# Kernel tuning notes

Hardware: AMD Instinct MI355X
Metric: run time of the kernel (lower is better)

## Reference

```python
import jax, jax.numpy as jnp
import numpy as np

EMBED = 768
HEADS = 12
D_K = EMBED // HEADS  # 64


def setup_inputs() -> dict:
    key = jax.random.key(0)
    ks = jax.random.split(key, 9)
    w_scale = EMBED ** -0.5
    inp = {
        "x": jax.random.normal(ks[0], (128, 256, 1, EMBED), dtype=jnp.float32),
        "Wq": jax.random.normal(ks[1], (EMBED, EMBED), dtype=jnp.float32) * w_scale,
        "bq": jax.random.normal(ks[2], (EMBED,), dtype=jnp.float32) * 0.02,
        "Wk": jax.random.normal(ks[3], (EMBED, EMBED), dtype=jnp.float32) * w_scale,
        "bk": jax.random.normal(ks[4], (EMBED,), dtype=jnp.float32) * 0.02,
        "Wv": jax.random.normal(ks[5], (EMBED, EMBED), dtype=jnp.float32) * w_scale,
        "bv": jax.random.normal(ks[6], (EMBED,), dtype=jnp.float32) * 0.02,
        "Wo": jax.random.normal(ks[7], (EMBED, EMBED), dtype=jnp.float32) * w_scale,
        "bo": jax.random.normal(ks[8], (EMBED,), dtype=jnp.float32) * 0.02,
    }
    return inp


def reference(x, Wq, bq, Wk, bk, Wv, bv, Wo, bo):
    # x: (n_rows r, n_cols i/j, batch n, embed)
    R, C, B, E = x.shape
    H, Dk = HEADS, D_K
    # tied-row scaling: d_k^{-1/2} / sqrt(n_rows)
    scaling = (Dk ** -0.5) / np.sqrt(R).astype(np.float32)

    q = (x @ Wq.T + bq).reshape(R, C, B, H, Dk) * scaling
    k = (x @ Wk.T + bk).reshape(R, C, B, H, Dk)
    v = (x @ Wv.T + bv).reshape(R, C, B, H, Dk)

    # scores summed over rows r and head dim d -> (h, n, i, j)
    scores = jnp.einsum('rinhd,rjnhd->hnij', q, k)
    probs = jax.nn.softmax(scores, axis=-1)  # dropout p=0 -> identity

    # shared attention applied per row
    c = jnp.einsum('hnij,rjnhd->rinhd', probs, v).reshape(R, C, B, E)
    out = c @ Wo.T + bo
    return (out, probs)
```

## Files before the change

kernel.cpp:

```cpp
#include <hip/hip_runtime.h>
#include <math.h>

typedef short bf16x8 __attribute__((ext_vector_type(8)));
typedef float f32x4 __attribute__((ext_vector_type(4)));
typedef unsigned short ushort8 __attribute__((ext_vector_type(8)));
typedef unsigned short ushort4v __attribute__((ext_vector_type(4)));

constexpr int R = 128, Cc = 256, E = 768, H = 12;
constexpr int M = R * Cc;
constexpr size_t TOK = (size_t)M * E;

__device__ __forceinline__ unsigned short f2b(float f) {
  unsigned int u = __float_as_uint(f);
  u += 0x7fff + ((u >> 16) & 1);
  return (unsigned short)(u >> 16);
}

__device__ __forceinline__ void ldst16(const unsigned short* g, unsigned short* l) {
  __builtin_amdgcn_global_load_lds(
      (const __attribute__((address_space(1))) unsigned int*)g,
      (__attribute__((address_space(3))) unsigned int*)l, 16, 0, 0);
}

__global__ __launch_bounds__(256) void cvt_bf16(const float* __restrict__ in,
                                                unsigned short* __restrict__ out,
                                                int n8) {
  int i = blockIdx.x * 256 + threadIdx.x;
  if (i >= n8) return;
  const float4* p = (const float4*)in;
  float4 a = p[2 * i], b = p[2 * i + 1];
  ushort8 o;
  o[0] = f2b(a.x); o[1] = f2b(a.y); o[2] = f2b(a.z); o[3] = f2b(a.w);
  o[4] = f2b(b.x); o[5] = f2b(b.y); o[6] = f2b(b.z); o[7] = f2b(b.w);
  ((ushort8*)out)[i] = o;
}

__global__ __launch_bounds__(256) void cvt_w4(const float* __restrict__ W0,
                                              const float* __restrict__ W1,
                                              const float* __restrict__ W2,
                                              const float* __restrict__ W3,
                                              unsigned short* __restrict__ out) {
  const int region = blockIdx.x / 288;
  const int i = (blockIdx.x % 288) * 256 + threadIdx.x;
  if (i >= 73728) return;
  const float* src = region == 0 ? W0 : (region == 1 ? W1 : (region == 2 ? W2 : W3));
  const float4* p = (const float4*)src;
  float4 a = p[2 * i], b = p[2 * i + 1];
  ushort8 o;
  o[0] = f2b(a.x); o[1] = f2b(a.y); o[2] = f2b(a.z); o[3] = f2b(a.w);
  o[4] = f2b(b.x); o[5] = f2b(b.y); o[6] = f2b(b.z); o[7] = f2b(b.w);
  ((ushort8*)(out + (size_t)region * 589824))[i] = o;
}

__device__ __forceinline__ void stage64(const unsigned short* __restrict__ A, int lda,
                                        const unsigned short* __restrict__ B, int ldb,
                                        int k0, unsigned short* As, unsigned short* Bs,
                                        int wv, int ln, int srow, int scol) {
#pragma unroll
  for (int t = 0; t < 4; ++t) {
    const int ch = wv * 4 + t;
    const int row = ch * 8 + srow;
    ldst16(A + (size_t)row * lda + k0 + scol, As + ch * 512 + ln * 8);
    ldst16(B + (size_t)row * ldb + k0 + scol, Bs + ch * 512 + ln * 8);
  }
}

__device__ __forceinline__ void gemm128(const unsigned short* __restrict__ A, int lda,
                                        const unsigned short* __restrict__ B, int ldb,
                                        int K, unsigned short* As, unsigned short* Bs,
                                        int wv, int ln, int wm, int wn,
                                        f32x4 (&acc)[4][4]) {
  const int srow = ln >> 3;
  const int scol = ((ln & 7) ^ srow) * 8;
  const int nt = K >> 6;
  stage64(A, lda, B, ldb, 0, As, Bs, wv, ln, srow, scol);
  if (nt > 1)
    stage64(A, lda, B, ldb, 64, As + 8192, Bs + 8192, wv, ln, srow, scol);
  for (int t = 0; t < nt; ++t) {
    const int cur = t & 1;
    if (t + 1 < nt) {
      asm volatile("s_waitcnt vmcnt(8)" ::: "memory");
    } else {
      asm volatile("s_waitcnt vmcnt(0)" ::: "memory");
    }
    __builtin_amdgcn_sched_barrier(0);
    __builtin_amdgcn_s_barrier();
    const unsigned short* Ab = As + cur * 8192;
    const unsigned short* Bb = Bs + cur * 8192;
    bf16x8 a[2][4], b[2][4];
    {
      const int rc0 = (((ln >> 4)) ^ (ln & 7)) * 8;
#pragma unroll
      for (int i = 0; i < 4; ++i)
        a[0][i] = *(const bf16x8*)(Ab + (wm + i * 16 + (ln & 15)) * 64 + rc0);
#pragma unroll
      for (int j = 0; j < 4; ++j)
        b[0][j] = *(const bf16x8*)(Bb + (wn + j * 16 + (ln & 15)) * 64 + rc0);
    }
    __builtin_amdgcn_sched_barrier(0);
    {
      const int rc1 = ((4 + (ln >> 4)) ^ (ln & 7)) * 8;
#pragma unroll
      for (int i = 0; i < 4; ++i)
        a[1][i] = *(const bf16x8*)(Ab + (wm + i * 16 + (ln & 15)) * 64 + rc1);
#pragma unroll
      for (int j = 0; j < 4; ++j)
        b[1][j] = *(const bf16x8*)(Bb + (wn + j * 16 + (ln & 15)) * 64 + rc1);
    }
    asm volatile("s_waitcnt lgkmcnt(8)" ::: "memory");
    __builtin_amdgcn_sched_barrier(0);
    __builtin_amdgcn_s_setprio(1);
#pragma unroll
    for (int i = 0; i < 4; ++i)
#pragma unroll
      for (int j = 0; j < 4; ++j)
        acc[i][j] = __builtin_amdgcn_mfma_f32_16x16x32_bf16(a[0][i], b[0][j],
                                                            acc[i][j], 0, 0, 0);
    __builtin_amdgcn_s_setprio(0);
    asm volatile("s_waitcnt lgkmcnt(0)" ::: "memory");
    __builtin_amdgcn_sched_barrier(0);
    __builtin_amdgcn_s_barrier();
    if (t + 2 < nt)
      stage64(A, lda, B, ldb, (t + 2) * 64, As + cur * 8192, Bs + cur * 8192,
              wv, ln, srow, scol);
    __builtin_amdgcn_s_setprio(1);
#pragma unroll
    for (int i = 0; i < 4; ++i)
#pragma unroll
      for (int j = 0; j < 4; ++j)
        acc[i][j] = __builtin_amdgcn_mfma_f32_16x16x32_bf16(a[1][i], b[1][j],
                                                            acc[i][j], 0, 0, 0);
    __builtin_amdgcn_s_setprio(0);
  }
}

__global__ __launch_bounds__(256) void qkv_proj(
    const unsigned short* __restrict__ A, const unsigned short* __restrict__ B,
    const float* __restrict__ bq, const float* __restrict__ bk,
    const float* __restrict__ bv, unsigned short* __restrict__ q2,
    unsigned short* __restrict__ k2, unsigned short* __restrict__ v3, float scaling) {
  __shared__ unsigned short As[2 * 128 * 64];
  __shared__ unsigned short Bs[2 * 128 * 64];
  const int tid = threadIdx.x, wv = tid >> 6, ln = tid & 63;
  const unsigned p = blockIdx.x + blockIdx.y * 18;
  const unsigned l = (p & 7) * 576 + (p >> 3);
  const int bx = l % 18, by = l / 18;
  const int n0 = bx * 128, m0 = by * 128;
  const int wm = (wv & 1) * 64, wn = (wv >> 1) * 64;
  f32x4 acc[4][4] = {};
  gemm128(A + (size_t)m0 * 768, 768, B + (size_t)n0 * 768, 768, 768,
          As, Bs, wv, ln, wm, wn, acc);

  const int region = bx / 6;
  const float* bias = region == 0 ? bq : (region == 1 ? bk : bv);
  const float sc = region == 0 ? scaling : 1.0f;
  const int nq0 = n0 - region * 768;
#pragma unroll
  for (int j = 0; j < 4; ++j) {
    const int np = nq0 + wn + j * 16 + (ln & 15);
    const int h = np >> 6, d = np & 63;
    const float bn = bias[np];
#pragma unroll
    for (int i = 0; i < 4; ++i) {
      const int mb = m0 + wm + i * 16 + (ln >> 4) * 4;
      if (region < 2) {
        unsigned short* dst = region == 0 ? q2 : k2;
#pragma unroll
        for (int r = 0; r < 4; ++r) {
          const int m = mb + r;
          const int ic = m & 255, rr = m >> 8;
          dst[(size_t)h * 2097152 + (size_t)ic * 8192 + rr * 64 + d] =
              f2b((acc[i][j][r] + bn) * sc);
        }
      } else {
        const int jc = mb & 255, rr = mb >> 8;
        ushort4v o;
#pragma unroll
        for (int r = 0; r < 4; ++r) o[r] = f2b(acc[i][j][r] + bn);
        *(ushort4v*)(v3 + (size_t)h * 2097152 + ((size_t)rr * 64 + d) * 256 + jc) = o;
      }
    }
  }
}

__global__ __launch_bounds__(256) void qk_gemm(const unsigned short* __restrict__ q2,
                                               const unsigned short* __restrict__ k2,
                                               float* __restrict__ Sp) {
  __shared__ unsigned short As[2 * 128 * 64];
  __shared__ unsigned short Bs[2 * 128 * 64];
  const int tid = threadIdx.x, wv = tid >> 6, ln = tid & 63;
  const int i0 = (blockIdx.x & 1) * 128, j0 = (blockIdx.x >> 1) * 128;
  const int h = blockIdx.y, kc = blockIdx.z;
  const int wm = (wv & 1) * 64, wn = (wv >> 1) * 64;
  f32x4 acc[4][4] = {};
  const unsigned short* Ap = q2 + (size_t)h * 2097152 + (size_t)i0 * 8192 + kc * 1024;
  const unsigned short* Bp = k2 + (size_t)h * 2097152 + (size_t)j0 * 8192 + kc * 1024;
  gemm128(Ap, 8192, Bp, 8192, 1024, As, Bs, wv, ln, wm, wn, acc);
  float* out = Sp + ((size_t)kc * H + h) * 65536;
#pragma unroll
  for (int j = 0; j < 4; ++j) {
    const int jj = j0 + wn + j * 16 + (ln & 15);
#pragma unroll
    for (int i = 0; i < 4; ++i)
#pragma unroll
      for (int r = 0; r < 4; ++r) {
        const int ii = i0 + wm + i * 16 + (ln >> 4) * 4 + r;
        out[(size_t)ii * 256 + jj] = acc[i][j][r];
      }
  }
}

__global__ __launch_bounds__(256) void softmax_k(const float* __restrict__ Sp,
                                                 float* __restrict__ P,
                                                 unsigned short* __restrict__ Pb) {
  const int row = blockIdx.x, j = threadIdx.x;
  const size_t stride = (size_t)H * Cc * Cc;
  const size_t base = (size_t)row * Cc + j;
  float s = 0.f;
#pragma unroll
  for (int c = 0; c < 8; ++c) s += Sp[base + c * stride];
  float m = s;
#pragma unroll
  for (int o = 32; o > 0; o >>= 1) m = fmaxf(m, __shfl_xor(m, o));
  __shared__ float sm[4], ss[4];
  const int wid = j >> 6, lane = j & 63;
  if (lane == 0) sm[wid] = m;
  __syncthreads();
  m = fmaxf(fmaxf(sm[0], sm[1]), fmaxf(sm[2], sm[3]));
  float e = expf(s - m);
  float t = e;
#pragma unroll
  for (int o = 32; o > 0; o >>= 1) t += __shfl_xor(t, o);
  if (lane == 0) ss[wid] = t;
  __syncthreads();
  t = ss[0] + ss[1] + ss[2] + ss[3];
  const float p = e / t;
  P[base] = p;
  Pb[base] = f2b(p);
}

__global__ __launch_bounds__(256) void pv_gemm(const unsigned short* __restrict__ P,
                                               const unsigned short* __restrict__ V,
                                               unsigned short* __restrict__ Co) {
  __shared__ unsigned short As[2 * 128 * 64];
  __shared__ unsigned short Bs[2 * 128 * 64];
  const int tid = threadIdx.x, wv = tid >> 6, ln = tid & 63;
  const unsigned p = blockIdx.x + blockIdx.y * 128;
  const unsigned l = (p & 7) * 192 + (p >> 3);
  const int bx = l & 127, h = l >> 7;
  const int i0 = (bx & 1) * 128, n0 = (bx >> 1) * 128;
  const int wm = (wv & 1) * 64, wn = (wv >> 1) * 64;
  f32x4 acc[4][4] = {};
  const unsigned short* Ap = P + (size_t)h * 65536 + (size_t)i0 * 256;
  const unsigned short* Bp = V + (size_t)h * 2097152 + (size_t)n0 * 256;
  gemm128(Ap, 256, Bp, 256, 256, As, Bs, wv, ln, wm, wn, acc);
#pragma unroll
  for (int j = 0; j < 4; ++j) {
    const int n = n0 + wn + j * 16 + (ln & 15);
    const int rr = n >> 6, d = n & 63;
#pragma unroll
    for (int i = 0; i < 4; ++i)
#pragma unroll
      for (int r = 0; r < 4; ++r) {
        const int ii = i0 + wm + i * 16 + (ln >> 4) * 4 + r;
        Co[((size_t)rr * 256 + ii) * 768 + h * 64 + d] = f2b(acc[i][j][r]);
      }
  }
}

__global__ __launch_bounds__(256) void o_proj(const unsigned short* __restrict__ A,
                                              const unsigned short* __restrict__ B,
                                              const float* __restrict__ bias,
                                              float* __restrict__ Y) {
  __shared__ unsigned short As[2 * 128 * 64];
  __shared__ unsigned short Bs[2 * 128 * 64];
  const int tid = threadIdx.x, wv = tid >> 6, ln = tid & 63;
  const unsigned p = blockIdx.x + blockIdx.y * 6;
  const unsigned l = (p & 7) * 192 + (p >> 3);
  const int bx = l % 6, by = l / 6;
  const int n0 = bx * 128, m0 = by * 128;
  const int wm = (wv & 1) * 64, wn = (wv >> 1) * 64;
  f32x4 acc[4][4] = {};
  gemm128(A + (size_t)m0 * 768, 768, B + (size_t)n0 * 768, 768, 768,
          As, Bs, wv, ln, wm, wn, acc);
#pragma unroll
  for (int j = 0; j < 4; ++j) {
    const int n = n0 + wn + j * 16 + (ln & 15);
    const float bn = bias[n];
#pragma unroll
    for (int i = 0; i < 4; ++i)
#pragma unroll
      for (int r = 0; r < 4; ++r) {
        const int m = m0 + wm + i * 16 + (ln >> 4) * 4 + r;
        Y[(size_t)m * 768 + n] = acc[i][j][r] + bn;
      }
  }
}

extern "C" void kernel_launch(void* const* d_in, const int* in_sizes, int n_in,
                              void* d_out, int out_size, void* d_ws, size_t ws_size,
                              hipStream_t stream) {
  const float* x  = (const float*)d_in[0];
  const float* Wq = (const float*)d_in[1];
  const float* bq = (const float*)d_in[2];
  const float* Wk = (const float*)d_in[3];
  const float* bk = (const float*)d_in[4];
  const float* Wv = (const float*)d_in[5];
  const float* bv = (const float*)d_in[6];
  const float* Wo = (const float*)d_in[7];
  const float* bo = (const float*)d_in[8];
  float* out = (float*)d_out;
  float* probs = out + TOK;

  char* ws = (char*)d_ws;
  unsigned short* x_bf  = (unsigned short*)(ws);
  unsigned short* q2    = (unsigned short*)(ws + 50331648);
  unsigned short* k2    = (unsigned short*)(ws + 100663296);
  unsigned short* v3    = (unsigned short*)(ws + 150994944);
  unsigned short* Wq_bf = (unsigned short*)(ws + 201326592);
  unsigned short* Wk_bf = Wq_bf + 589824;
  unsigned short* Wv_bf = Wk_bf + 589824;
  unsigned short* Wo_bf = Wv_bf + 589824;
  float* S_part         = (float*)(ws);
  unsigned short* P_bf  = (unsigned short*)(ws + 25165824);
  unsigned short* c_bf  = q2;

  const float scaling = 0.125f / sqrtf(128.f);

  cvt_bf16<<<12288, 256, 0, stream>>>(x, x_bf, 3145728);
  cvt_w4<<<1152, 256, 0, stream>>>(Wq, Wk, Wv, Wo, Wq_bf);

  qkv_proj<<<dim3(18, 256), 256, 0, stream>>>(x_bf, Wq_bf, bq, bk, bv,
                                              q2, k2, v3, scaling);

  qk_gemm<<<dim3(4, H, 8), 256, 0, stream>>>(q2, k2, S_part);
  softmax_k<<<H * Cc, 256, 0, stream>>>(S_part, probs, P_bf);
  pv_gemm<<<dim3(128, H), 256, 0, stream>>>(P_bf, v3, c_bf);

  o_proj<<<dim3(6, 256), 256, 0, stream>>>(c_bf, Wo_bf, bo, out);
}
```

Baseline: 505.0 us.

## Use 256x256 tiles with 512-thread blocks for projection and PV GEMMs

Adds a gemm256 path in which 8 waves compute a 256x256 output tile with a K-step of 32, double-buffered through global_load_lds. The QKV projection, PV and output projection kernels move to it, which doubles operand reuse per byte loaded and reduces the number of blocks. The older gemm128, still used by qk_gemm, is simplified so that all fragment loads complete before a single MFMA phase, dropping the split lgkmcnt overlap. Risks include higher register pressure with 32 accumulators per wave, fewer blocks for load balancing, and possible LDS bank conflicts from the new swizzle.

Result: slower. 528.5 us (+4.7%).

```diff
diff --git a/kernel.cpp b/kernel.cpp
--- a/kernel.cpp
+++ b/kernel.cpp
@@ -50,6 +50,62 @@
   o[0] = f2b(a.x); o[1] = f2b(a.y); o[2] = f2b(a.z); o[3] = f2b(a.w);
   o[4] = f2b(b.x); o[5] = f2b(b.y); o[6] = f2b(b.z); o[7] = f2b(b.w);
   ((ushort8*)(out + (size_t)region * 589824))[i] = o;
+}
+
+__device__ __forceinline__ void stage256(const unsigned short* __restrict__ A, int lda,
+                                         const unsigned short* __restrict__ B, int ldb,
+                                         int k0, unsigned short* As, unsigned short* Bs,
+                                         int tid) {
+  const int r0 = tid >> 2;
+  const int g = ((tid & 3) ^ ((tid >> 3) & 3)) * 8;
+#pragma unroll
+  for (int o = 0; o < 2; ++o) {
+    const int row = o * 128 + r0;
+    ldst16(A + (size_t)row * lda + k0 + g, As + o * 4096 + tid * 8);
+    ldst16(B + (size_t)row * ldb + k0 + g, Bs + o * 4096 + tid * 8);
+  }
+}
+
+__device__ __forceinline__ void gemm256(const unsigned short* __restrict__ A, int lda,
+                                        const unsigned short* __restrict__ B, int ldb,
+                                        int K, unsigned short* As, unsigned short* Bs,
+                                        int tid, int ln, int wm, int wn,
+                                        f32x4 (&acc)[8][4]) {
+  const int nt = K >> 5;
+  stage256(A, lda, B, ldb, 0, As, Bs, tid);
+  stage256(A, lda, B, ldb, 32, As + 8192, Bs + 8192, tid);
+  const int rc = ((ln >> 4) ^ ((ln >> 1) & 3)) * 8;
+  for (int t = 0; t < nt; ++t) {
+    const int cur = t & 1;
+    if (t + 1 < nt) {
+      asm volatile("s_waitcnt vmcnt(4)" ::: "memory");
+    } else {
+      asm volatile("s_waitcnt vmcnt(0)" ::: "memory");
+    }
+    __builtin_amdgcn_sched_barrier(0);
+    __builtin_amdgcn_s_barrier();
+    const unsigned short* Ab = As + cur * 8192;
+    const unsigned short* Bb = Bs + cur * 8192;
+    bf16x8 a[8], b[4];
+#pragma unroll
+    for (int i = 0; i < 8; ++i)
+      a[i] = *(const bf16x8*)(Ab + (wm + i * 16 + (ln & 15)) * 32 + rc);
+#pragma unroll
+    for (int j = 0; j < 4; ++j)
+      b[j] = *(const bf16x8*)(Bb + (wn + j * 16 + (ln & 15)) * 32 + rc);
+    asm volatile("s_waitcnt lgkmcnt(0)" ::: "memory");
+    __builtin_amdgcn_sched_barrier(0);
+    __builtin_amdgcn_s_barrier();
+    if (t + 2 < nt)
+      stage256(A, lda, B, ldb, (t + 2) * 32, As + cur * 8192, Bs + cur * 8192, tid);
+    __builtin_amdgcn_s_setprio(1);
+#pragma unroll
+    for (int i = 0; i < 8; ++i)
+#pragma unroll
+      for (int j = 0; j < 4; ++j)
+        acc[i][j] = __builtin_amdgcn_mfma_f32_16x16x32_bf16(a[i], b[j], acc[i][j], 0, 0, 0);
+    __builtin_amdgcn_s_setprio(0);
+  }
 }
 
 __device__ __forceinline__ void stage64(const unsigned short* __restrict__ A, int lda,
@@ -88,96 +144,73 @@
     const unsigned short* Ab = As + cur * 8192;
     const unsigned short* Bb = Bs + cur * 8192;
     bf16x8 a[2][4], b[2][4];
-    {
-      const int rc0 = (((ln >> 4)) ^ (ln & 7)) * 8;
+#pragma unroll
+    for (int dk = 0; dk < 2; ++dk) {
+      const int rc = ((dk * 4 + (ln >> 4)) ^ (ln & 7)) * 8;
 #pragma unroll
       for (int i = 0; i < 4; ++i)
-        a[0][i] = *(const bf16x8*)(Ab + (wm + i * 16 + (ln & 15)) * 64 + rc0);
+        a[dk][i] = *(const bf16x8*)(Ab + (wm + i * 16 + (ln & 15)) * 64 + rc);
 #pragma unroll
       for (int j = 0; j < 4; ++j)
-        b[0][j] = *(const bf16x8*)(Bb + (wn + j * 16 + (ln & 15)) * 64 + rc0);
+        b[dk][j] = *(const bf16x8*)(Bb + (wn + j * 16 + (ln & 15)) * 64 + rc);
     }
-    __builtin_amdgcn_sched_barrier(0);
-    {
-      const int rc1 = ((4 + (ln >> 4)) ^ (ln & 7)) * 8;
-#pragma unroll
-      for (int i = 0; i < 4; ++i)
-        a[1][i] = *(const bf16x8*)(Ab + (wm + i * 16 + (ln & 15)) * 64 + rc1);
-#pragma unroll
-      for (int j = 0; j < 4; ++j)
-        b[1][j] = *(const bf16x8*)(Bb + (wn + j * 16 + (ln & 15)) * 64 + rc1);
-    }
-    asm volatile("s_waitcnt lgkmcnt(8)" ::: "memory");
-    __builtin_amdgcn_sched_barrier(0);
-    __builtin_amdgcn_s_setprio(1);
-#pragma unroll
-    for (int i = 0; i < 4; ++i)
-#pragma unroll
-      for (int j = 0; j < 4; ++j)
-        acc[i][j] = __builtin_amdgcn_mfma_f32_16x16x32_bf16(a[0][i], b[0][j],
-                                                            acc[i][j], 0, 0, 0);
-    __builtin_amdgcn_s_setprio(0);
     asm volatile("s_waitcnt lgkmcnt(0)" ::: "memory");
     __builtin_amdgcn_sched_barrier(0);
     __builtin_amdgcn_s_barrier();
     if (t + 2 < nt)
       stage64(A, lda, B, ldb, (t + 2) * 64, As + cur * 8192, Bs + cur * 8192,
               wv, ln, srow, scol);
-    __builtin_amdgcn_s_setprio(1);
-#pragma unroll
-    for (int i = 0; i < 4; ++i)
-#pragma unroll
-      for (int j = 0; j < 4; ++j)
-        acc[i][j] = __builtin_amdgcn_mfma_f32_16x16x32_bf16(a[1][i], b[1][j],
-                                                            acc[i][j], 0, 0, 0);
-    __builtin_amdgcn_s_setprio(0);
-  }
-}
-
-__global__ __launch_bounds__(256) void qkv_proj(
+#pragma unroll
+    for (int dk = 0; dk < 2; ++dk)
+#pragma unroll
+      for (int i = 0; i < 4; ++i)
+#pragma unroll
+        for (int j = 0; j < 4; ++j)
+          acc[i][j] = __builtin_amdgcn_mfma_f32_16x16x32_bf16(a[dk][i], b[dk][j],
+                                                              acc[i][j], 0, 0, 0);
+  }
+}
+
+__global__ __launch_bounds__(512, 2) void qkv_proj(
     const unsigned short* __restrict__ A, const unsigned short* __restrict__ B,
     const float* __restrict__ bq, const float* __restrict__ bk,
     const float* __restrict__ bv, unsigned short* __restrict__ q2,
     unsigned short* __restrict__ k2, unsigned short* __restrict__ v3, float scaling) {
-  __shared__ unsigned short As[2 * 128 * 64];
-  __shared__ unsigned short Bs[2 * 128 * 64];
+  __shared__ unsigned short As[16384];
+  __shared__ unsigned short Bs[16384];
   const int tid = threadIdx.x, wv = tid >> 6, ln = tid & 63;
-  const unsigned p = blockIdx.x + blockIdx.y * 18;
-  const unsigned l = (p & 7) * 576 + (p >> 3);
-  const int bx = l % 18, by = l / 18;
-  const int n0 = bx * 128, m0 = by * 128;
-  const int wm = (wv & 1) * 64, wn = (wv >> 1) * 64;
-  f32x4 acc[4][4] = {};
-  gemm128(A + (size_t)m0 * 768, 768, B + (size_t)n0 * 768, 768, 768,
-          As, Bs, wv, ln, wm, wn, acc);
-
-  const int region = bx / 6;
+  const int wr = wv >> 2, wc = wv & 3;
+  const unsigned p = blockIdx.x + blockIdx.y * 9;
+  const unsigned l = (p & 7) * 144 + (p >> 3);
+  const int bx = l % 9, by = l / 9;
+  const int n0 = bx * 256;
+  f32x4 acc[8][4] = {};
+  gemm256(A + (size_t)by * 256 * 768, 768, B + (size_t)n0 * 768, 768, 768,
+          As, Bs, tid, ln, wr * 128, wc * 64, acc);
+
+  const int region = bx / 3;
   const float* bias = region == 0 ? bq : (region == 1 ? bk : bv);
   const float sc = region == 0 ? scaling : 1.0f;
   const int nq0 = n0 - region * 768;
 #pragma unroll
   for (int j = 0; j < 4; ++j) {
-    const int np = nq0 + wn + j * 16 + (ln & 15);
+    const int np = nq0 + wc * 64 + j * 16 + (ln & 15);
     const int h = np >> 6, d = np & 63;
     const float bn = bias[np];
 #pragma unroll
-    for (int i = 0; i < 4; ++i) {
-      const int mb = m0 + wm + i * 16 + (ln >> 4) * 4;
+    for (int i = 0; i < 8; ++i) {
+      const int mloc = wr * 128 + i * 16 + (ln >> 4) * 4;
       if (region < 2) {
         unsigned short* dst = region == 0 ? q2 : k2;
 #pragma unroll
-        for (int r = 0; r < 4; ++r) {
-          const int m = mb + r;
-          const int ic = m & 255, rr = m >> 8;
-          dst[(size_t)h * 2097152 + (size_t)ic * 8192 + rr * 64 + d] =
+        for (int r = 0; r < 4; ++r)
+          dst[(size_t)h * 2097152 + (size_t)(mloc + r) * 8192 + by * 64 + d] =
               f2b((acc[i][j][r] + bn) * sc);
-        }
       } else {
-        const int jc = mb & 255, rr = mb >> 8;
         ushort4v o;
 #pragma unroll
         for (int r = 0; r < 4; ++r) o[r] = f2b(acc[i][j][r] + bn);
-        *(ushort4v*)(v3 + (size_t)h * 2097152 + ((size_t)rr * 64 + d) * 256 + jc) = o;
+        *(ushort4v*)(v3 + (size_t)h * 2097152 + ((size_t)by * 64 + d) * 256 + mloc) = o;
       }
     }
   }
@@ -239,59 +272,58 @@
   Pb[base] = f2b(p);
 }
 
-__global__ __launch_bounds__(256) void pv_gemm(const unsigned short* __restrict__ P,
-                                               const unsigned short* __restrict__ V,
-                                               unsigned short* __restrict__ Co) {
-  __shared__ unsigned short As[2 * 128 * 64];
-  __shared__ unsigned short Bs[2 * 128 * 64];
+__global__ __launch_bounds__(512, 2) void pv_gemm(const unsigned short* __restrict__ P,
+                                                  const unsigned short* __restrict__ V,
+                                                  unsigned short* __restrict__ Co) {
+  __shared__ unsigned short As[16384];
+  __shared__ unsigned short Bs[16384];
   const int tid = threadIdx.x, wv = tid >> 6, ln = tid & 63;
-  const unsigned p = blockIdx.x + blockIdx.y * 128;
-  const unsigned l = (p & 7) * 192 + (p >> 3);
-  const int bx = l & 127, h = l >> 7;
-  const int i0 = (bx & 1) * 128, n0 = (bx >> 1) * 128;
-  const int wm = (wv & 1) * 64, wn = (wv >> 1) * 64;
-  f32x4 acc[4][4] = {};
-  const unsigned short* Ap = P + (size_t)h * 65536 + (size_t)i0 * 256;
-  const unsigned short* Bp = V + (size_t)h * 2097152 + (size_t)n0 * 256;
-  gemm128(Ap, 256, Bp, 256, 256, As, Bs, wv, ln, wm, wn, acc);
+  const int wr = wv >> 2, wc = wv & 3;
+  const unsigned p = blockIdx.x + blockIdx.y * 32;
+  const unsigned l = (p & 7) * 48 + (p >> 3);
+  const int bx = l & 31, h = l >> 5;
+  const int n0 = bx * 256;
+  f32x4 acc[8][4] = {};
+  gemm256(P + (size_t)h * 65536, 256, V + (size_t)h * 2097152 + (size_t)n0 * 256, 256,
+          256, As, Bs, tid, ln, wr * 128, wc * 64, acc);
 #pragma unroll
   for (int j = 0; j < 4; ++j) {
-    const int n = n0 + wn + j * 16 + (ln & 15);
+    const int n = n0 + wc * 64 + j * 16 + (ln & 15);
     const int rr = n >> 6, d = n & 63;
 #pragma unroll
-    for (int i = 0; i < 4; ++i)
+    for (int i = 0; i < 8; ++i)
 #pragma unroll
       for (int r = 0; r < 4; ++r) {
-        const int ii = i0 + wm + i * 16 + (ln >> 4) * 4 + r;
+        const int ii = wr * 128 + i * 16 + (ln >> 4) * 4 + r;
         Co[((size_t)rr * 256 + ii) * 768 + h * 64 + d] = f2b(acc[i][j][r]);
       }
   }
 }
 
-__global__ __launch_bounds__(256) void o_proj(const unsigned short* __restrict__ A,
-                                              const unsigned short* __restrict__ B,
-                                              const float* __restrict__ bias,
-                                              float* __restrict__ Y) {
-  __shared__ unsigned short As[2 * 128 * 64];
-  __shared__ unsigned short Bs[2 * 128 * 64];
+__global__ __launch_bounds__(512, 2) void o_proj(const unsigned short* __restrict__ A,
+                                                 const unsigned short* __restrict__ B,
+                                                 const float* __restrict__ bias,
+                                                 float* __restrict__ Y) {
+  __shared__ unsigned short As[16384];
+  __shared__ unsigned short Bs[16384];
   const int tid = threadIdx.x, wv = tid >> 6, ln = tid & 63;
-  const unsigned p = blockIdx.x + blockIdx.y * 6;
-  const unsigned l = (p & 7) * 192 + (p >> 3);
-  const int bx = l % 6, by = l / 6;
-  const int n0 = bx * 128, m0 = by * 128;
-  const int wm = (wv & 1) * 64, wn = (wv >> 1) * 64;
-  f32x4 acc[4][4] = {};
-  gemm128(A + (size_t)m0 * 768, 768, B + (size_t)n0 * 768, 768, 768,
-          As, Bs, wv, ln, wm, wn, acc);
+  const int wr = wv >> 2, wc = wv & 3;
+  const unsigned p = blockIdx.x + blockIdx.y * 3;
+  const unsigned l = (p & 7) * 48 + (p >> 3);
+  const int bx = l % 3, by = l / 3;
+  const int n0 = bx * 256, m0 = by * 256;
+  f32x4 acc[8][4] = {};
+  gemm256(A + (size_t)m0 * 768, 768, B + (size_t)n0 * 768, 768, 768,
+          As, Bs, tid, ln, wr * 128, wc * 64, acc);
 #pragma unroll
   for (int j = 0; j < 4; ++j) {
-    const int n = n0 + wn + j * 16 + (ln & 15);
+    const int n = n0 + wc * 64 + j * 16 + (ln & 15);
     const float bn = bias[n];
 #pragma unroll
-    for (int i = 0; i < 4; ++i)
+    for (int i = 0; i < 8; ++i)
 #pragma unroll
       for (int r = 0; r < 4; ++r) {
-        const int m = m0 + wm + i * 16 + (ln >> 4) * 4 + r;
+        const int m = m0 + wr * 128 + i * 16 + (ln >> 4) * 4 + r;
         Y[(size_t)m * 768 + n] = acc[i][j][r] + bn;
       }
   }
@@ -318,9 +350,7 @@
   unsigned short* k2    = (unsigned short*)(ws + 100663296);
   unsigned short* v3    = (unsigned short*)(ws + 150994944);
   unsigned short* Wq_bf = (unsigned short*)(ws + 201326592);
-  unsigned short* Wk_bf = Wq_bf + 589824;
-  unsigned short* Wv_bf = Wk_bf + 589824;
-  unsigned short* Wo_bf = Wv_bf + 589824;
+  unsigned short* Wo_bf = Wq_bf + 3 * 589824;
   float* S_part         = (float*)(ws);
   unsigned short* P_bf  = (unsigned short*)(ws + 25165824);
   unsigned short* c_bf  = q2;
@@ -330,12 +360,12 @@
   cvt_bf16<<<12288, 256, 0, stream>>>(x, x_bf, 3145728);
   cvt_w4<<<1152, 256, 0, stream>>>(Wq, Wk, Wv, Wo, Wq_bf);
 
-  qkv_proj<<<dim3(18, 256), 256, 0, stream>>>(x_bf, Wq_bf, bq, bk, bv,
-                                              q2, k2, v3, scaling);
+  qkv_proj<<<dim3(9, 128), 512, 0, stream>>>(x_bf, Wq_bf, bq, bk, bv,
+                                             q2, k2, v3, scaling);
 
   qk_gemm<<<dim3(4, H, 8), 256, 0, stream>>>(q2, k2, S_part);
   softmax_k<<<H * Cc, 256, 0, stream>>>(S_part, probs, P_bf);
-  pv_gemm<<<dim3(128, H), 256, 0, stream>>>(P_bf, v3, c_bf);
-
-  o_proj<<<dim3(6, 256), 256, 0, stream>>>(c_bf, Wo_bf, bo, out);
-}
+  pv_gemm<<<dim3(32, H), 512, 0, stream>>>(P_bf, v3, c_bf);
+
+  o_proj<<<dim3(3, 128), 512, 0, stream>>>(c_bf, Wo_bf, bo, out);
+}
```

## Use 256x256 tiles with 8-wave phased pipeline for QKV projection GEMM

Applied to the files above, without the earlier changes.

Replaces the 128x128 QKV projection GEMM with a 256x256 tile computed by 512 threads (8 waves). Its schedule splits each K-step into four phases that interleave LDS reads, async global-to-LDS staging and MFMA blocks. The larger tile raises arithmetic intensity and cuts redundant global loads of x and weights. The cost is higher register and LDS use, with one block per CU. The shared gemm128 helper is also simplified to issue all LDS reads before a single barrier, so the two MFMA halves are no longer overlapped with the staging; this affects the other GEMMs.

Result: faster. 473.8 us (-6.2%).

```diff
diff --git a/kernel.cpp b/kernel.cpp
--- a/kernel.cpp
+++ b/kernel.cpp
@@ -50,6 +50,143 @@
   o[0] = f2b(a.x); o[1] = f2b(a.y); o[2] = f2b(a.z); o[3] = f2b(a.w);
   o[4] = f2b(b.x); o[5] = f2b(b.y); o[6] = f2b(b.z); o[7] = f2b(b.w);
   ((ushort8*)(out + (size_t)region * 589824))[i] = o;
+}
+
+__device__ __forceinline__ void stage_half(const unsigned short* __restrict__ G,
+                                           int k0, unsigned short* lbase,
+                                           int wv, int ln) {
+  const int chunk = ((ln & 7) ^ (ln >> 3)) * 8;
+  const int r0 = wv * 8 + (ln >> 3);
+#pragma unroll
+  for (int l = 0; l < 2; ++l) {
+    const int row = l * 64 + r0;
+    ldst16(G + (size_t)row * 768 + k0 + chunk, lbase + l * 4096 + wv * 512 + ln * 8);
+  }
+}
+
+__device__ __forceinline__ void gemm256_8ph(
+    const unsigned short* __restrict__ At,
+    const unsigned short* __restrict__ Bt,
+    unsigned short* As, unsigned short* Bs,
+    int wv, int ln, int wm, int wn, f32x4 (&acc)[8][4]) {
+#pragma unroll
+  for (int t = 0; t < 2; ++t) {
+    stage_half(Bt, t * 64, Bs + t * 16384, wv, ln);
+    stage_half(Bt + (size_t)128 * 768, t * 64, Bs + t * 16384 + 8192, wv, ln);
+    stage_half(At, t * 64, As + t * 16384, wv, ln);
+    stage_half(At + (size_t)128 * 768, t * 64, As + t * 16384 + 8192, wv, ln);
+  }
+  const int rw = (ln & 15);
+  const int rx = ln & 7;
+  for (int it = 0; it < 6; ++it) {
+#pragma unroll
+    for (int hi = 0; hi < 2; ++hi) {
+      const int tc = 2 * it + hi;
+      const unsigned short* Ab = As + (tc & 1) * 16384;
+      const unsigned short* Bb = Bs + (tc & 1) * 16384;
+      unsigned short* Asn = As + ((tc + 1) & 1) * 16384;
+      unsigned short* Bsn = Bs + ((tc + 1) & 1) * 16384;
+      unsigned short* Bs2 = Bs + (tc & 1) * 16384;
+      const int k1 = (tc + 1) * 64, k2 = (tc + 2) * 64;
+      const bool st01 = (hi == 0) ? (it >= 1) : (it <= 4);
+      const bool st3 = (it <= 4);
+      bf16x8 a0[4][2], a1[4][2], b0[2][2], b1[2][2];
+      if (hi == 0) {
+        if (it == 0) { asm volatile("s_waitcnt vmcnt(8)" ::: "memory"); }
+        else         { asm volatile("s_waitcnt vmcnt(2)" ::: "memory"); }
+      } else {
+        if (it < 5)  { asm volatile("s_waitcnt vmcnt(2)" ::: "memory"); }
+        else         { asm volatile("s_waitcnt vmcnt(0)" ::: "memory"); }
+      }
+      __builtin_amdgcn_sched_barrier(0);
+      __builtin_amdgcn_s_barrier();
+#pragma unroll
+      for (int i = 0; i < 4; ++i)
+#pragma unroll
+        for (int kk = 0; kk < 2; ++kk)
+          a0[i][kk] = *(const bf16x8*)(Ab + (wm + i * 16 + rw) * 64 +
+                                       (((kk * 4 + (ln >> 4)) ^ rx) * 8));
+#pragma unroll
+      for (int j = 0; j < 2; ++j)
+#pragma unroll
+        for (int kk = 0; kk < 2; ++kk)
+          b0[j][kk] = *(const bf16x8*)(Bb + (wn + j * 16 + rw) * 64 +
+                                       (((kk * 4 + (ln >> 4)) ^ rx) * 8));
+      if (st01) stage_half(Bt + (size_t)128 * 768, k1, Bsn + 8192, wv, ln);
+      asm volatile("s_waitcnt lgkmcnt(0)" ::: "memory");
+      __builtin_amdgcn_sched_barrier(0);
+      __builtin_amdgcn_s_setprio(1);
+#pragma unroll
+      for (int i = 0; i < 4; ++i)
+#pragma unroll
+        for (int j = 0; j < 2; ++j)
+#pragma unroll
+          for (int kk = 0; kk < 2; ++kk)
+            acc[i][j] = __builtin_amdgcn_mfma_f32_16x16x32_bf16(a0[i][kk], b0[j][kk],
+                                                                acc[i][j], 0, 0, 0);
+      __builtin_amdgcn_s_setprio(0);
+      __builtin_amdgcn_s_barrier();
+#pragma unroll
+      for (int i = 0; i < 4; ++i)
+#pragma unroll
+        for (int kk = 0; kk < 2; ++kk)
+          a1[i][kk] = *(const bf16x8*)(Ab + (wm + (i + 4) * 16 + rw) * 64 +
+                                       (((kk * 4 + (ln >> 4)) ^ rx) * 8));
+      if (st01) stage_half(At, k1, Asn, wv, ln);
+      asm volatile("s_waitcnt lgkmcnt(0)" ::: "memory");
+      __builtin_amdgcn_sched_barrier(0);
+      __builtin_amdgcn_s_setprio(1);
+#pragma unroll
+      for (int i = 0; i < 4; ++i)
+#pragma unroll
+        for (int j = 0; j < 2; ++j)
+#pragma unroll
+          for (int kk = 0; kk < 2; ++kk)
+            acc[i + 4][j] = __builtin_amdgcn_mfma_f32_16x16x32_bf16(a1[i][kk], b0[j][kk],
+                                                                    acc[i + 4][j], 0, 0, 0);
+      __builtin_amdgcn_s_setprio(0);
+      __builtin_amdgcn_s_barrier();
+#pragma unroll
+      for (int j = 0; j < 2; ++j)
+#pragma unroll
+        for (int kk = 0; kk < 2; ++kk)
+          b1[j][kk] = *(const bf16x8*)(Bb + (wn + (j + 2) * 16 + rw) * 64 +
+                                       (((kk * 4 + (ln >> 4)) ^ rx) * 8));
+      if (st01) stage_half(At + (size_t)128 * 768, k1, Asn + 8192, wv, ln);
+      asm volatile("s_waitcnt lgkmcnt(0)" ::: "memory");
+      __builtin_amdgcn_sched_barrier(0);
+      __builtin_amdgcn_s_setprio(1);
+#pragma unroll
+      for (int i = 0; i < 4; ++i)
+#pragma unroll
+        for (int j = 0; j < 2; ++j)
+#pragma unroll
+          for (int kk = 0; kk < 2; ++kk)
+            acc[i + 4][j + 2] = __builtin_amdgcn_mfma_f32_16x16x32_bf16(
+                a1[i][kk], b1[j][kk], acc[i + 4][j + 2], 0, 0, 0);
+      __builtin_amdgcn_s_setprio(0);
+      __builtin_amdgcn_s_barrier();
+#pragma unroll
+      for (int i = 0; i < 4; ++i)
+#pragma unroll
+        for (int kk = 0; kk < 2; ++kk)
+          a0[i][kk] = *(const bf16x8*)(Ab + (wm + i * 16 + rw) * 64 +
+                                       (((kk * 4 + (ln >> 4)) ^ rx) * 8));
+      if (st3) stage_half(Bt, k2, Bs2, wv, ln);
+      asm volatile("s_waitcnt lgkmcnt(0)" ::: "memory");
+      __builtin_amdgcn_sched_barrier(0);
+      __builtin_amdgcn_s_setprio(1);
+#pragma unroll
+      for (int i = 0; i < 4; ++i)
+#pragma unroll
+        for (int j = 0; j < 2; ++j)
+#pragma unroll
+          for (int kk = 0; kk < 2; ++kk)
+            acc[i][j + 2] = __builtin_amdgcn_mfma_f32_16x16x32_bf16(
+                a0[i][kk], b1[j][kk], acc[i][j + 2], 0, 0, 0);
+      __builtin_amdgcn_s_setprio(0);
+    }
+  }
 }
 
 __device__ __forceinline__ void stage64(const unsigned short* __restrict__ A, int lda,
@@ -88,96 +225,73 @@
     const unsigned short* Ab = As + cur * 8192;
     const unsigned short* Bb = Bs + cur * 8192;
     bf16x8 a[2][4], b[2][4];
-    {
-      const int rc0 = (((ln >> 4)) ^ (ln & 7)) * 8;
-#pragma unroll
-      for (int i = 0; i < 4; ++i)
-        a[0][i] = *(const bf16x8*)(Ab + (wm + i * 16 + (ln & 15)) * 64 + rc0);
+#pragma unroll
+    for (int dk = 0; dk < 2; ++dk) {
+      const int rc = ((dk * 4 + (ln >> 4)) ^ (ln & 7)) * 8;
+#pragma unroll
+      for (int i = 0; i < 4; ++i)
+        a[dk][i] = *(const bf16x8*)(Ab + (wm + i * 16 + (ln & 15)) * 64 + rc);
 #pragma unroll
       for (int j = 0; j < 4; ++j)
-        b[0][j] = *(const bf16x8*)(Bb + (wn + j * 16 + (ln & 15)) * 64 + rc0);
+        b[dk][j] = *(const bf16x8*)(Bb + (wn + j * 16 + (ln & 15)) * 64 + rc);
     }
-    __builtin_amdgcn_sched_barrier(0);
-    {
-      const int rc1 = ((4 + (ln >> 4)) ^ (ln & 7)) * 8;
-#pragma unroll
-      for (int i = 0; i < 4; ++i)
-        a[1][i] = *(const bf16x8*)(Ab + (wm + i * 16 + (ln & 15)) * 64 + rc1);
-#pragma unroll
-      for (int j = 0; j < 4; ++j)
-        b[1][j] = *(const bf16x8*)(Bb + (wn + j * 16 + (ln & 15)) * 64 + rc1);
-    }
-    asm volatile("s_waitcnt lgkmcnt(8)" ::: "memory");
-    __builtin_amdgcn_sched_barrier(0);
-    __builtin_amdgcn_s_setprio(1);
-#pragma unroll
-    for (int i = 0; i < 4; ++i)
-#pragma unroll
-      for (int j = 0; j < 4; ++j)
-        acc[i][j] = __builtin_amdgcn_mfma_f32_16x16x32_bf16(a[0][i], b[0][j],
-                                                            acc[i][j], 0, 0, 0);
-    __builtin_amdgcn_s_setprio(0);
     asm volatile("s_waitcnt lgkmcnt(0)" ::: "memory");
     __builtin_amdgcn_sched_barrier(0);
     __builtin_amdgcn_s_barrier();
     if (t + 2 < nt)
       stage64(A, lda, B, ldb, (t + 2) * 64, As + cur * 8192, Bs + cur * 8192,
               wv, ln, srow, scol);
-    __builtin_amdgcn_s_setprio(1);
-#pragma unroll
-    for (int i = 0; i < 4; ++i)
-#pragma unroll
-      for (int j = 0; j < 4; ++j)
-        acc[i][j] = __builtin_amdgcn_mfma_f32_16x16x32_bf16(a[1][i], b[1][j],
-                                                            acc[i][j], 0, 0, 0);
-    __builtin_amdgcn_s_setprio(0);
-  }
-}
-
-__global__ __launch_bounds__(256) void qkv_proj(
+#pragma unroll
+    for (int dk = 0; dk < 2; ++dk)
+#pragma unroll
+      for (int i = 0; i < 4; ++i)
+#pragma unroll
+        for (int j = 0; j < 4; ++j)
+          acc[i][j] = __builtin_amdgcn_mfma_f32_16x16x32_bf16(a[dk][i], b[dk][j],
+                                                              acc[i][j], 0, 0, 0);
+  }
+}
+
+__global__ __launch_bounds__(512, 1) void qkv_proj(
     const unsigned short* __restrict__ A, const unsigned short* __restrict__ B,
     const float* __restrict__ bq, const float* __restrict__ bk,
     const float* __restrict__ bv, unsigned short* __restrict__ q2,
     unsigned short* __restrict__ k2, unsigned short* __restrict__ v3, float scaling) {
-  __shared__ unsigned short As[2 * 128 * 64];
-  __shared__ unsigned short Bs[2 * 128 * 64];
+  __shared__ unsigned short As[2 * 16384];
+  __shared__ unsigned short Bs[2 * 16384];
   const int tid = threadIdx.x, wv = tid >> 6, ln = tid & 63;
-  const unsigned p = blockIdx.x + blockIdx.y * 18;
-  const unsigned l = (p & 7) * 576 + (p >> 3);
-  const int bx = l % 18, by = l / 18;
-  const int n0 = bx * 128, m0 = by * 128;
-  const int wm = (wv & 1) * 64, wn = (wv >> 1) * 64;
-  f32x4 acc[4][4] = {};
-  gemm128(A + (size_t)m0 * 768, 768, B + (size_t)n0 * 768, 768, 768,
-          As, Bs, wv, ln, wm, wn, acc);
-
-  const int region = bx / 6;
+  const int wr = wv >> 2, wc = wv & 3;
+  const unsigned p = blockIdx.x + blockIdx.y * 9;
+  const unsigned l = (p & 7) * 144 + (p >> 3);
+  const int bx = l % 9, by = l / 9;
+  const int n0 = bx * 256;
+  f32x4 acc[8][4] = {};
+  gemm256_8ph(A + (size_t)by * 256 * 768, B + (size_t)n0 * 768,
+              As, Bs, wv, ln, wr * 128, wc * 64, acc);
+
+  const int region = bx / 3;
   const float* bias = region == 0 ? bq : (region == 1 ? bk : bv);
   const float sc = region == 0 ? scaling : 1.0f;
   const int nq0 = n0 - region * 768;
 #pragma unroll
   for (int j = 0; j < 4; ++j) {
-    const int np = nq0 + wn + j * 16 + (ln & 15);
+    const int np = nq0 + wc * 64 + j * 16 + (ln & 15);
     const int h = np >> 6, d = np & 63;
     const float bn = bias[np];
 #pragma unroll
-    for (int i = 0; i < 4; ++i) {
-      const int mb = m0 + wm + i * 16 + (ln >> 4) * 4;
+    for (int i = 0; i < 8; ++i) {
+      const int mloc = wr * 128 + i * 16 + (ln >> 4) * 4;
       if (region < 2) {
         unsigned short* dst = region == 0 ? q2 : k2;
 #pragma unroll
-        for (int r = 0; r < 4; ++r) {
-          const int m = mb + r;
-          const int ic = m & 255, rr = m >> 8;
-          dst[(size_t)h * 2097152 + (size_t)ic * 8192 + rr * 64 + d] =
+        for (int r = 0; r < 4; ++r)
+          dst[(size_t)h * 2097152 + (size_t)(mloc + r) * 8192 + by * 64 + d] =
               f2b((acc[i][j][r] + bn) * sc);
-        }
       } else {
-        const int jc = mb & 255, rr = mb >> 8;
         ushort4v o;
 #pragma unroll
         for (int r = 0; r < 4; ++r) o[r] = f2b(acc[i][j][r] + bn);
-        *(ushort4v*)(v3 + (size_t)h * 2097152 + ((size_t)rr * 64 + d) * 256 + jc) = o;
+        *(ushort4v*)(v3 + (size_t)h * 2097152 + ((size_t)by * 64 + d) * 256 + mloc) = o;
       }
     }
   }
@@ -318,9 +432,7 @@
   unsigned short* k2    = (unsigned short*)(ws + 100663296);
   unsigned short* v3    = (unsigned short*)(ws + 150994944);
   unsigned short* Wq_bf = (unsigned short*)(ws + 201326592);
-  unsigned short* Wk_bf = Wq_bf + 589824;
-  unsigned short* Wv_bf = Wk_bf + 589824;
-  unsigned short* Wo_bf = Wv_bf + 589824;
+  unsigned short* Wo_bf = Wq_bf + 3 * 589824;
   float* S_part         = (float*)(ws);
   unsigned short* P_bf  = (unsigned short*)(ws + 25165824);
   unsigned short* c_bf  = q2;
@@ -330,8 +442,8 @@
   cvt_bf16<<<12288, 256, 0, stream>>>(x, x_bf, 3145728);
   cvt_w4<<<1152, 256, 0, stream>>>(Wq, Wk, Wv, Wo, Wq_bf);
 
-  qkv_proj<<<dim3(18, 256), 256, 0, stream>>>(x_bf, Wq_bf, bq, bk, bv,
-                                              q2, k2, v3, scaling);
+  qkv_proj<<<dim3(9, 128), 512, 0, stream>>>(x_bf, Wq_bf, bq, bk, bv,
+                                             q2, k2, v3, scaling);
 
   qk_gemm<<<dim3(4, H, 8), 256, 0, stream>>>(q2, k2, S_part);
   softmax_k<<<H * Cc, 256, 0, stream>>>(S_part, probs, P_bf);
```
